# Optimization experiments

Measured on AMD Instinct MI355X. Metric: run time of the kernel, lower is better.

The kernel has to match this reference:

```python
import jax, jax.numpy as jnp
import numpy as np

N_ITERS = 5
LAMBDA = 0.01


def _skew(v):
    # (..., 3) -> (..., 3, 3)
    x, y, z = v[..., 0], v[..., 1], v[..., 2]
    zero = jnp.zeros_like(x)
    return jnp.stack([
        jnp.stack([zero, -z, y], -1),
        jnp.stack([z, zero, -x], -1),
        jnp.stack([-y, x, zero], -1)], -2)


def _so3exp(w):
    # Rodrigues' formula, safe at theta ~ 0.
    th = jnp.sqrt(jnp.sum(w * w) + 1e-24)
    W = _skew(w)
    A = jnp.sin(th) / th
    B = (1.0 - jnp.cos(th)) / (th * th)
    return jnp.eye(3, dtype=w.dtype) + A * W + B * (W @ W)


def setup_inputs():
    key = jax.random.key(0)
    ks = jax.random.split(key, 6)
    N, C, Himg, Wimg = 32768, 128, 480, 640
    xy = jax.random.normal(ks[0], (N, 2), jnp.float32) * 1.5
    z = jax.random.uniform(ks[1], (N, 1), jnp.float32, minval=4.0, maxval=10.0)
    pts3D = jnp.concatenate([xy, z], -1)  # points in front of camera
    feature_ref = jax.random.normal(ks[2], (N, C), jnp.float32)
    feature_map_query = jax.random.normal(ks[3], (C, Himg, Wimg), jnp.float32)
    feature_grad_x = jax.random.normal(ks[4], (C, Himg, Wimg), jnp.float32) * 0.1
    feature_grad_y = jax.random.normal(ks[5], (C, Himg, Wimg), jnp.float32) * 0.1
    K = jnp.array([[600.0, 0.0, 320.0], [0.0, 600.0, 240.0], [0.0, 0.0, 1.0]], jnp.float32)
    R_init = jnp.eye(3, dtype=jnp.float32)
    t_init = jnp.array([0.05, -0.03, 0.02], jnp.float32)
    return {"pts3D": pts3D, "feature_ref": feature_ref,
            "feature_map_query": feature_map_query,
            "feature_grad_x": feature_grad_x, "feature_grad_y": feature_grad_y,
            "K": K, "R_init": R_init, "t_init": t_init,
            "im_width": 640, "im_height": 480}


def reference(pts3D, feature_ref, feature_map_query, feature_grad_x, feature_grad_y,
              K, R_init, t_init, im_width, im_height):
    C, fmH, fmW = feature_map_query.shape
    dt_ = pts3D.dtype
    eye3 = jnp.eye(3, dtype=dt_)
    fx, fy = K[0, 0], K[1, 1]
    R, t = R_init, t_init
    for _ in range(N_ITERS):
        p3d = pts3D @ R.T + t                                  # (N,3) camera frame
        ph = p3d @ K.T
        p2d = jnp.round(ph[:, :2] / ph[:, 2:3]).astype(jnp.int32) - 1  # (N,2) = (x,y)
        mask = ((p2d[:, 0] >= 0) & (p2d[:, 1] >= 0) &
                (p2d[:, 0] < im_width) & (p2d[:, 1] < im_height)).astype(dt_)
        # indexing_ with flipped points: row from y, col from x, scaled to map size
        rows = jnp.clip(jnp.floor(p2d[:, 1].astype(dt_) * fmH / im_height).astype(jnp.int32), 0, fmH - 1)
        cols = jnp.clip(jnp.floor(p2d[:, 0].astype(dt_) * fmW / im_width).astype(jnp.int32), 0, fmW - 1)
        e = feature_map_query[:, rows, cols].T - feature_ref   # (N,C) feature error
        J_f_px = jnp.stack([feature_grad_x[:, rows, cols].T,
                            feature_grad_y[:, rows, cols].T], -1)  # (N,C,2)
        x, y, z = p3d[:, 0], p3d[:, 1], p3d[:, 2]
        zinv = 1.0 / z
        zero = jnp.zeros_like(x)
        # pinhole projection Jacobian (N,2,3)
        J_px_p = jnp.stack([fx * zinv, zero, -fx * x * zinv * zinv,
                            zero, fy * zinv, -fy * y * zinv * zinv], -1).reshape(-1, 2, 3)
        # point-to-pose Jacobian [I | -skew(p)] (N,3,6)
        J_p_T = jnp.concatenate([jnp.broadcast_to(eye3, (p3d.shape[0], 3, 3)), -_skew(p3d)], -1)
        # masked full Jacobian (N,C,6); mask replaces boolean row selection
        J = jnp.einsum('nci,nij,njk->nck', J_f_px, J_px_p, J_p_T) * mask[:, None, None]
        g = jnp.einsum('nck,nc->k', J, e)                      # (6,)
        H = jnp.einsum('nci,ncj->ij', J, J)                    # (6,6)
        H = H + LAMBDA * jnp.diag(jnp.diag(H) + 1e-9)          # LM damping
        delta = -jnp.linalg.solve(H, g)                        # GN/LM step
        dR = _so3exp(delta[3:])
        R = dR @ R
        t = dR @ t + delta[:3]
    return R, t
```

## Files before the change

### kernel.cpp

```cpp
#include <hip/hip_runtime.h>
#include <math.h>

#define NPTS   32768
#define CCH    128
#define FMH    480
#define FMW    640
#define PLANE  (FMH*FMW)
#define IMW    640
#define IMH    480
#define PPB    32
#define NBLKA  (NPTS/PPB)
#define NPART  27
#define MSTR   8
#define ROWB   256
#define SCL    200.0f
#define INVS   0.005f

typedef float vfloat4 __attribute__((ext_vector_type(4)));

__device__ __forceinline__ float f4e(const float4& v, int i){
    return i==0 ? v.x : i==1 ? v.y : i==2 ? v.z : v.w;
}

__device__ __forceinline__ int q8(float v){
    return (int)rintf(fminf(fmaxf(v*SCL, -127.f), 127.f));
}

__device__ __forceinline__ unsigned pack2(float a0,float b0,float a1,float b1){
    return (unsigned)(q8(a0)&255) | ((unsigned)(q8(b0)&255)<<8)
         | ((unsigned)(q8(a1)&255)<<16) | ((unsigned)(q8(b1)&255)<<24);
}

__device__ __forceinline__ float sb2f(unsigned u, int i){
    return (float)((int)(u << (24 - 8*i)) >> 24);
}

__device__ __forceinline__ void dec4(unsigned u, float rA, float rB,
                                     float& dx, float& dy){
    dx = fmaf(sb2f(u,0), rA, dx);
    dy = fmaf(sb2f(u,1), rA, dy);
    dx = fmaf(sb2f(u,2), rB, dx);
    dy = fmaf(sb2f(u,3), rB, dy);
}

__device__ __forceinline__ float4 ntload4(const float* p){
    vfloat4 v = __builtin_nontemporal_load(reinterpret_cast<const vfloat4*>(p));
    return make_float4(v.x, v.y, v.z, v.w);
}

__global__ __launch_bounds__(256)
void pnp_prep(const float* __restrict__ fmap,
              const float* __restrict__ gxm,
              const float* __restrict__ gym,
              unsigned char* __restrict__ gQ,
              float* __restrict__ maps8)
{
    __shared__ float spart[4][5][64];
    const int tid = threadIdx.x;
    const int pq  = (tid & 15) * 4;
    const int cqp = tid >> 4;
    const int w   = tid >> 6;
    const size_t p0 = (size_t)blockIdx.x * 64;

    float acc[5][4];
    #pragma unroll
    for (int m=0;m<5;m++)
        #pragma unroll
        for (int i=0;i<4;i++) acc[m][i]=0.f;

    #pragma unroll
    for (int rep=0; rep<2; ++rep){
        const int c0 = cqp*8 + rep*4;
        float4 gxv[4], gyv[4], fmv[4];
        #pragma unroll
        for (int j=0;j<4;j++){
            const size_t off = (size_t)(c0+j)*PLANE + p0 + pq;
            gxv[j] = ntload4(gxm  + off);
            gyv[j] = ntload4(gym  + off);
            fmv[j] = ntload4(fmap + off);
        }
        #pragma unroll
        for (int i=0;i<4;i++){
            float a[4], b[4];
            #pragma unroll
            for (int j=0;j<4;j++){
                a[j] = f4e(gxv[j], i);
                b[j] = f4e(gyv[j], i);
                const float f = f4e(fmv[j], i);
                acc[0][i] = fmaf(a[j], f, acc[0][i]);
                acc[1][i] = fmaf(b[j], f, acc[1][i]);
                acc[2][i] = fmaf(a[j], a[j], acc[2][i]);
                acc[3][i] = fmaf(a[j], b[j], acc[3][i]);
                acc[4][i] = fmaf(b[j], b[j], acc[4][i]);
            }
            uint2 st;
            st.x = pack2(a[0], b[0], a[1], b[1]);
            st.y = pack2(a[2], b[2], a[3], b[3]);
            const size_t byteoff = (p0 + pq + i)*ROWB + (size_t)cqp*16 + rep*8;
            *reinterpret_cast<uint2*>(gQ + byteoff) = st;
        }
    }

    const bool lo16 = ((tid >> 4) & 3) == 0;
    #pragma unroll
    for (int m=0;m<5;m++){
        #pragma unroll
        for (int i=0;i<4;i++){
            float v = acc[m][i];
            v += __shfl_xor(v, 16);
            v += __shfl_xor(v, 32);
            if (lo16) spart[w][m][pq+i] = v;
        }
    }
    __syncthreads();

    if (tid < 64){
        const size_t pix = p0 + tid;
        const float m0 = spart[0][0][tid]+spart[1][0][tid]+spart[2][0][tid]+spart[3][0][tid];
        const float m1 = spart[0][1][tid]+spart[1][1][tid]+spart[2][1][tid]+spart[3][1][tid];
        const float m2 = spart[0][2][tid]+spart[1][2][tid]+spart[2][2][tid]+spart[3][2][tid];
        const float m3 = spart[0][3][tid]+spart[1][3][tid]+spart[2][3][tid]+spart[3][3][tid];
        const float m4 = spart[0][4][tid]+spart[1][4][tid]+spart[2][4][tid]+spart[3][4][tid];
        float4 v4; v4.x=m0; v4.y=m1; v4.z=m2; v4.w=m3;
        *reinterpret_cast<float4*>(&maps8[pix*MSTR]) = v4;
        maps8[pix*MSTR + 4] = m4;
    }
}

__global__ __launch_bounds__(256)
void pnp_accum2(const float* __restrict__ pts3D,
                const float* __restrict__ fref,
                const unsigned char* __restrict__ gQ,
                const float* __restrict__ maps8,
                const float* __restrict__ Kmat,
                const float* __restrict__ Rsrc,
                const float* __restrict__ tsrc,
                float* __restrict__ partials)
{
    const int tid = threadIdx.x;
    const int g   = tid & 7;
    const int pl  = tid >> 3;
    const int n   = blockIdx.x * PPB + pl;

    const float4* rp = reinterpret_cast<const float4*>(fref + (size_t)n*CCH + g*16);
    const float4 r0 = rp[0];
    const float4 r1 = rp[1];
    const float4 r2 = rp[2];
    const float4 r3 = rp[3];

    const float R00=Rsrc[0],R01=Rsrc[1],R02=Rsrc[2];
    const float R10=Rsrc[3],R11=Rsrc[4],R12=Rsrc[5];
    const float R20=Rsrc[6],R21=Rsrc[7],R22=Rsrc[8];
    const float t0=tsrc[0],t1=tsrc[1],t2=tsrc[2];
    const float K00=Kmat[0],K01=Kmat[1],K02=Kmat[2];
    const float K10=Kmat[3],K11=Kmat[4],K12=Kmat[5];
    const float K20=Kmat[6],K21=Kmat[7],K22=Kmat[8];
    const float fx=K00, fy=K11;

    const float px=pts3D[n*3+0], py=pts3D[n*3+1], pz=pts3D[n*3+2];
    const float x = R00*px + R01*py + R02*pz + t0;
    const float y = R10*px + R11*py + R12*pz + t1;
    const float z = R20*px + R21*py + R22*pz + t2;
    const float phx = K00*x + K01*y + K02*z;
    const float phy = K10*x + K11*y + K12*z;
    const float phz = K20*x + K21*y + K22*z;
    const int p2x = (int)rintf(phx/phz) - 1;
    const int p2y = (int)rintf(phy/phz) - 1;
    const bool inb = (p2x>=0) && (p2y>=0) && (p2x<IMW) && (p2y<IMH);
    const int pix = inb ? (p2y*FMW + p2x) : 0;

    float dx=0.f, dy=0.f;
    if (inb) {
        const uint4* gp =
            reinterpret_cast<const uint4*>(gQ + (size_t)pix*ROWB + g*32);
        const uint4 q0 = gp[0];
        const uint4 q1 = gp[1];
        dec4(q0.x, r0.x, r0.y, dx, dy);
        dec4(q0.y, r0.z, r0.w, dx, dy);
        dec4(q0.z, r1.x, r1.y, dx, dy);
        dec4(q0.w, r1.z, r1.w, dx, dy);
        dec4(q1.x, r2.x, r2.y, dx, dy);
        dec4(q1.y, r2.z, r2.w, dx, dy);
        dec4(q1.z, r3.x, r3.y, dx, dy);
        dec4(q1.w, r3.z, r3.w, dx, dy);
        dx *= INVS; dy *= INVS;
    }
    #pragma unroll
    for (int d=1; d<8; d<<=1){
        dx += __shfl_xor(dx, d);
        dy += __shfl_xor(dy, d);
    }

    float v[NPART];
    #pragma unroll
    for (int i=0;i<NPART;i++) v[i]=0.f;
    if (inb) {
        const float4 m03 = *reinterpret_cast<const float4*>(&maps8[(size_t)pix*MSTR]);
        const float  m4  = maps8[(size_t)pix*MSTR + 4];
        const float sx  = m03.x - dx;
        const float sy  = m03.y - dy;
        const float gxx = m03.z;
        const float gxy = m03.w;
        const float gyy = m4;

        const float zi = 1.f/z;
        const float a0 = fx*zi;
        const float b0 = -fx*x*zi*zi;
        const float c1 = fy*zi;
        const float d1 = -fy*y*zi*zi;
        const float A0[6] = {a0, 0.f, b0, b0*y, a0*z - b0*x, -a0*y};
        const float A1[6] = {0.f, c1, d1, -c1*z + d1*y, -d1*x, c1*x};
        #pragma unroll
        for (int i=0;i<6;i++) v[i] = A0[i]*sx + A1[i]*sy;
        int idx=6;
        #pragma unroll
        for (int i=0;i<6;i++){
            #pragma unroll
            for (int j=i;j<6;j++){
                v[idx] = gxx*A0[i]*A0[j]
                       + gxy*(A0[i]*A1[j]+A1[i]*A0[j])
                       + gyy*A1[i]*A1[j];
                idx++;
            }
        }
    }

    __shared__ float wpart[4][NPART];
    const int wid  = tid >> 6;
    const int lane = tid & 63;
    #pragma unroll
    for (int i=0;i<NPART;i++){
        float vv = v[i];
        vv += __shfl_xor(vv, 8);
        vv += __shfl_xor(vv, 16);
        vv += __shfl_xor(vv, 32);
        if (lane==0) wpart[wid][i]=vv;
    }
    __syncthreads();
    if (tid < NPART){
        partials[(size_t)tid*NBLKA + blockIdx.x] =
            wpart[0][tid]+wpart[1][tid]+wpart[2][tid]+wpart[3][tid];
    }
}

__global__ void pnp_solve(const float* __restrict__ partials,
                          const float* __restrict__ Rsrc,
                          const float* __restrict__ tsrc,
                          float* __restrict__ RtWs,
                          float* __restrict__ outp)
{
    __shared__ double red[NPART];
    const int t = threadIdx.x;
    if (t < NPART*8){
        const int col = t >> 3;
        const int k   = t & 7;
        const float4* p4 =
            reinterpret_cast<const float4*>(partials + (size_t)col*NBLKA) + k*32;
        double s = 0.0;
        #pragma unroll 4
        for (int i=0;i<32;i++){
            const float4 v = p4[i];
            s += (double)v.x + (double)v.y + (double)v.z + (double)v.w;
        }
        s += __shfl_xor(s, 1);
        s += __shfl_xor(s, 2);
        s += __shfl_xor(s, 4);
        if (k==0) red[col] = s;
    }
    __syncthreads();
    if (t==0){
        double gv[6]; double H[6][6];
        for (int i=0;i<6;i++) gv[i]=red[i];
        int idx=6;
        for (int i=0;i<6;i++)
            for (int j=i;j<6;j++){
                H[i][j]=red[idx]; H[j][i]=red[idx]; idx++;
            }
        for (int i=0;i<6;i++) H[i][i] += 0.01*(H[i][i] + 1e-9);

        double M[6][6], b[6];
        for (int i=0;i<6;i++){ b[i]=gv[i]; for (int j=0;j<6;j++) M[i][j]=H[i][j]; }
        for (int c=0;c<6;c++){
            int piv=c; double mx=fabs(M[c][c]);
            for (int r=c+1;r<6;r++){ double av=fabs(M[r][c]); if (av>mx){mx=av;piv=r;} }
            if (piv!=c){
                for (int j=c;j<6;j++){ double tmp=M[c][j]; M[c][j]=M[piv][j]; M[piv][j]=tmp; }
                double tb=b[c]; b[c]=b[piv]; b[piv]=tb;
            }
            const double inv = 1.0/M[c][c];
            for (int r=c+1;r<6;r++){
                const double f = M[r][c]*inv;
                for (int j=c;j<6;j++) M[r][j] -= f*M[c][j];
                b[r] -= f*b[c];
            }
        }
        double xs[6];
        for (int r=5;r>=0;r--){
            double s2=b[r];
            for (int j=r+1;j<6;j++) s2 -= M[r][j]*xs[j];
            xs[r]=s2/M[r][r];
        }
        double delta[6];
        for (int i=0;i<6;i++) delta[i] = -xs[i];

        const double wx=delta[3], wy=delta[4], wz=delta[5];
        const double th = sqrt(wx*wx+wy*wy+wz*wz + 1e-24);
        const double Ath = sin(th)/th;
        const double Bth = (1.0-cos(th))/(th*th);
        const double W[3][3] = {{0.0,-wz,wy},{wz,0.0,-wx},{-wy,wx,0.0}};
        double W2[3][3];
        for (int i=0;i<3;i++) for (int j=0;j<3;j++){
            double s2=0; for (int k2=0;k2<3;k2++) s2 += W[i][k2]*W[k2][j];
            W2[i][j]=s2;
        }
        double dR[3][3];
        for (int i=0;i<3;i++) for (int j=0;j<3;j++)
            dR[i][j] = (i==j?1.0:0.0) + Ath*W[i][j] + Bth*W2[i][j];

        double Ro[3][3];
        for (int i=0;i<3;i++) for (int j=0;j<3;j++) Ro[i][j]=(double)Rsrc[i*3+j];
        const double to0=(double)tsrc[0], to1=(double)tsrc[1], to2=(double)tsrc[2];

        double Rn[3][3], tn[3];
        for (int i=0;i<3;i++){
            for (int j=0;j<3;j++){
                double s2=0; for (int k2=0;k2<3;k2++) s2 += dR[i][k2]*Ro[k2][j];
                Rn[i][j]=s2;
            }
            tn[i] = dR[i][0]*to0 + dR[i][1]*to1 + dR[i][2]*to2 + delta[i];
        }
        for (int i=0;i<3;i++) for (int j=0;j<3;j++){
            RtWs[i*3+j] = (float)Rn[i][j];
            outp[i*3+j] = (float)Rn[i][j];
        }
        for (int i=0;i<3;i++){ RtWs[9+i]=(float)tn[i]; outp[9+i]=(float)tn[i]; }
    }
}

extern "C" void kernel_launch(void* const* d_in, const int* in_sizes, int n_in,
                              void* d_out, int out_size, void* d_ws, size_t ws_size,
                              hipStream_t stream)
{
    const float* pts   = (const float*)d_in[0];
    const float* fref  = (const float*)d_in[1];
    const float* fmap  = (const float*)d_in[2];
    const float* gxm   = (const float*)d_in[3];
    const float* gym   = (const float*)d_in[4];
    const float* Kmat  = (const float*)d_in[5];
    const float* Rin   = (const float*)d_in[6];
    const float* tin   = (const float*)d_in[7];
    float* outp = (float*)d_out;

    float* partials = (float*)d_ws;
    float* RtWs  = partials + (size_t)NPART*NBLKA;
    float* maps8 = RtWs + 12;
    unsigned char* gQ = reinterpret_cast<unsigned char*>(maps8 + (size_t)MSTR*PLANE);

    pnp_prep<<<PLANE/64, 256, 0, stream>>>(fmap, gxm, gym, gQ, maps8);

    const float* Rs = Rin;
    const float* ts = tin;
    for (int it=0; it<5; ++it){
        pnp_accum2<<<NBLKA, 256, 0, stream>>>(pts, fref, gQ, maps8,
                                              Kmat, Rs, ts, partials);
        pnp_solve<<<1, 256, 0, stream>>>(partials, Rs, ts, RtWs, outp);
        Rs = RtWs; ts = RtWs + 9;
    }
}
```

Baseline: 205.1 us.

## Assign two threads per point instead of eight in accumulation kernel

Each block now covers 128 points instead of 32. Each point is handled by 2 threads, and each thread processes 64 channels with wide loads and four independent accumulators. This cuts the cross-lane shuffles per point for the dot product, and it cuts the number of block partials that the solve kernel has to reduce. In exchange, each thread holds many more registers, which can lower occupancy. The per-point Hessian work is also spread over fewer redundant lanes, but the final reduction needs extra shuffle stages.

```diff
diff --git a/kernel.cpp b/kernel.cpp
--- a/kernel.cpp
+++ b/kernel.cpp
@@ -8,7 +8,7 @@
 #define PLANE  (FMH*FMW)
 #define IMW    640
 #define IMH    480
-#define PPB    32
+#define PPB    128
 #define NBLKA  (NPTS/PPB)
 #define NPART  27
 #define MSTR   8
@@ -138,15 +138,14 @@
                 float* __restrict__ partials)
 {
     const int tid = threadIdx.x;
-    const int g   = tid & 7;
-    const int pl  = tid >> 3;
+    const int g   = tid & 1;
+    const int pl  = tid >> 1;
     const int n   = blockIdx.x * PPB + pl;
 
-    const float4* rp = reinterpret_cast<const float4*>(fref + (size_t)n*CCH + g*16);
-    const float4 r0 = rp[0];
-    const float4 r1 = rp[1];
-    const float4 r2 = rp[2];
-    const float4 r3 = rp[3];
+    const float4* rp = reinterpret_cast<const float4*>(fref + (size_t)n*CCH + g*64);
+    float4 r[16];
+    #pragma unroll
+    for (int i=0;i<16;i++) r[i] = rp[i];
 
     const float R00=Rsrc[0],R01=Rsrc[1],R02=Rsrc[2];
     const float R10=Rsrc[3],R11=Rsrc[4],R12=Rsrc[5];
@@ -172,24 +171,25 @@
     float dx=0.f, dy=0.f;
     if (inb) {
         const uint4* gp =
-            reinterpret_cast<const uint4*>(gQ + (size_t)pix*ROWB + g*32);
-        const uint4 q0 = gp[0];
-        const uint4 q1 = gp[1];
-        dec4(q0.x, r0.x, r0.y, dx, dy);
-        dec4(q0.y, r0.z, r0.w, dx, dy);
-        dec4(q0.z, r1.x, r1.y, dx, dy);
-        dec4(q0.w, r1.z, r1.w, dx, dy);
-        dec4(q1.x, r2.x, r2.y, dx, dy);
-        dec4(q1.y, r2.z, r2.w, dx, dy);
-        dec4(q1.z, r3.x, r3.y, dx, dy);
-        dec4(q1.w, r3.z, r3.w, dx, dy);
-        dx *= INVS; dy *= INVS;
-    }
-    #pragma unroll
-    for (int d=1; d<8; d<<=1){
-        dx += __shfl_xor(dx, d);
-        dy += __shfl_xor(dy, d);
-    }
+            reinterpret_cast<const uint4*>(gQ + (size_t)pix*ROWB + g*128);
+        uint4 q[8];
+        #pragma unroll
+        for (int i=0;i<8;i++) q[i] = gp[i];
+        float dxa[4] = {0.f,0.f,0.f,0.f};
+        float dya[4] = {0.f,0.f,0.f,0.f};
+        #pragma unroll
+        for (int i=0;i<8;i++){
+            const int c = i & 3;
+            dec4(q[i].x, r[2*i].x,   r[2*i].y,   dxa[c], dya[c]);
+            dec4(q[i].y, r[2*i].z,   r[2*i].w,   dxa[c], dya[c]);
+            dec4(q[i].z, r[2*i+1].x, r[2*i+1].y, dxa[c], dya[c]);
+            dec4(q[i].w, r[2*i+1].z, r[2*i+1].w, dxa[c], dya[c]);
+        }
+        dx = ((dxa[0]+dxa[1]) + (dxa[2]+dxa[3])) * INVS;
+        dy = ((dya[0]+dya[1]) + (dya[2]+dya[3])) * INVS;
+    }
+    dx += __shfl_xor(dx, 1);
+    dy += __shfl_xor(dy, 1);
 
     float v[NPART];
     #pragma unroll
@@ -231,6 +231,8 @@
     #pragma unroll
     for (int i=0;i<NPART;i++){
         float vv = v[i];
+        vv += __shfl_xor(vv, 2);
+        vv += __shfl_xor(vv, 4);
         vv += __shfl_xor(vv, 8);
         vv += __shfl_xor(vv, 16);
         vv += __shfl_xor(vv, 32);
@@ -255,10 +257,10 @@
         const int col = t >> 3;
         const int k   = t & 7;
         const float4* p4 =
-            reinterpret_cast<const float4*>(partials + (size_t)col*NBLKA) + k*32;
+            reinterpret_cast<const float4*>(partials + (size_t)col*NBLKA) + k*8;
         double s = 0.0;
         #pragma unroll 4
-        for (int i=0;i<32;i++){
+        for (int i=0;i<8;i++){
             const float4 v = p4[i];
             s += (double)v.x + (double)v.y + (double)v.z + (double)v.w;
         }
```

Result: slower. 210.5 us (+2.6%).
